# Optimization experiments

Measured on AMD Instinct MI355X. Metric: run time of the kernel, lower is better.

The kernel has to match this reference:

```python
import jax, jax.numpy as jnp
import numpy as np

WS = 7  # window size


def _rel_pos_index(ws):
    coords = np.stack(np.meshgrid(np.arange(ws), np.arange(ws), indexing='ij')).reshape(2, -1)
    rel = (coords[:, :, None] - coords[:, None, :]).transpose(1, 2, 0)  # (N,N,2)
    rel[..., 0] += ws - 1
    rel[..., 1] += ws - 1
    rel[..., 0] *= 2 * ws - 1
    return jnp.asarray(rel.sum(-1))  # (N,N) int


def setup_inputs() -> dict:
    key = jax.random.key(0)
    ks = jax.random.split(key, 10)
    B, DIM, H, W, NH = 16, 256, 56, 56, 8
    HD = DIM // NH
    x = jax.random.normal(ks[0], (B, DIM, H, W), jnp.float32)
    qkv_w = jax.random.normal(ks[1], (DIM, 3 * DIM), jnp.float32) * 0.02
    qkv_b = jnp.zeros((3 * DIM,), jnp.float32)
    fc_w = jax.random.normal(ks[2], (9, 3 * NH), jnp.float32) * 0.1
    fc_b = jnp.zeros((9,), jnp.float32)
    base = np.zeros((9, 3, 3), np.float32)
    for i in range(9):
        base[i, i // 3, i % 3] = 1.0
    dep_w = jnp.asarray(np.broadcast_to(base, (DIM, 9, 3, 3)).copy()) \
        + jax.random.normal(ks[3], (DIM, 9, 3, 3), jnp.float32) * 0.01
    proj_w = jax.random.normal(ks[4], (DIM, DIM), jnp.float32) * 0.02
    proj_b = jnp.zeros((DIM,), jnp.float32)
    rpb_table = jax.random.normal(ks[5], ((2 * WS - 1) * (2 * WS - 1), NH), jnp.float32) * 0.02
    rate1 = jnp.full((1,), 0.5, jnp.float32)
    rate2 = jnp.full((1,), 0.5, jnp.float32)
    return dict(x=x, qkv_w=qkv_w, qkv_b=qkv_b, fc_w=fc_w, fc_b=fc_b, dep_w=dep_w,
                proj_w=proj_w, proj_b=proj_b, rpb_table=rpb_table, rate1=rate1, rate2=rate2)


def reference(x, qkv_w, qkv_b, fc_w, fc_b, dep_w, proj_w, proj_b, rpb_table, rate1, rate2):
    B, DIM, H, W = x.shape
    NH = fc_w.shape[1] // 3
    HD = DIM // NH
    N = WS * WS
    xp = jnp.transpose(x, (0, 2, 3, 1))              # (B,H,W,C)
    qkv = xp @ qkv_w + qkv_b                          # (B,H,W,3C)

    # ----- conv branch -----
    f_all = qkv.reshape(B, H * W, 3 * NH, HD)         # (B,HW,3NH,HD)
    fc_out = jnp.einsum('oc,bncd->bnod', fc_w, f_all) + fc_b[None, None, :, None]  # (B,HW,9,HD)
    # torch channel layout: (B, HD, 9, HW) -> (B, 9*HD, H, W) with hd-major ordering
    f_conv = jnp.transpose(fc_out, (0, 3, 2, 1)).reshape(B, 9 * HD, H, W)
    out_conv = jax.lax.conv_general_dilated(
        f_conv, dep_w, window_strides=(1, 1), padding=((1, 1), (1, 1)),
        feature_group_count=HD, dimension_numbers=('NCHW', 'OIHW', 'NCHW'))  # (B,C,H,W)
    out_conv = jnp.transpose(out_conv, (0, 2, 3, 1))  # (B,H,W,C)

    # ----- window attention branch -----
    w = qkv.reshape(B, H // WS, WS, W // WS, WS, 3 * DIM)
    w = jnp.transpose(w, (0, 1, 3, 2, 4, 5)).reshape(-1, N, 3 * DIM)  # (B_,N,3C)
    B_ = w.shape[0]
    w = w.reshape(B_, N, 3, NH, HD)
    q, k, v = jnp.transpose(w, (2, 0, 3, 1, 4))       # each (B_,NH,N,HD)
    scale = HD ** -0.5
    attn = jnp.einsum('bhnd,bhmd->bhnm', q * scale, k)  # (B_,NH,N,N)
    idx = _rel_pos_index(WS)
    bias = jnp.transpose(rpb_table[idx.reshape(-1)].reshape(N, N, NH), (2, 0, 1))  # (NH,N,N)
    attn = jax.nn.softmax(attn + bias[None], axis=-1)
    o = jnp.einsum('bhnm,bhmd->bnhd', attn, v).reshape(B_, N, DIM)
    o = o @ proj_w.T + proj_b                          # torch Linear: y = x W^T + b
    o = o.reshape(B_, WS, WS, DIM)
    o = o.reshape(B, H // WS, W // WS, WS, WS, DIM)
    o = jnp.transpose(o, (0, 1, 3, 2, 4, 5)).reshape(B, H, W, DIM)

    out = rate1 * o + rate2 * out_conv
    return jnp.transpose(out, (0, 3, 1, 2))           # (B,C,H,W)
```

## Files before the change

kernel.cpp:

```cpp
#include <hip/hip_runtime.h>

#define BATCH 16
#define DIM 256
#define HH 56
#define WW 56
#define HWP 3136
#define M_TOT 50176
#define NQKV 768
#define NHEADS 8
#define HDIM 32
#define NWIN 49
#define QKV_BYTES   77070336ull
#define XT_OFF      77070336ull
#define XT_BYTES    25690112ull
#define WQT_OFF    102760448ull
#define PWB_OFF    103153664ull
#define FCONV_OFF  103284736ull

typedef float f32x4 __attribute__((ext_vector_type(4)));
typedef short short8 __attribute__((ext_vector_type(8)));
typedef unsigned short ushort4v __attribute__((ext_vector_type(4)));

__device__ __forceinline__ short f2bf(float f) {
    unsigned u = __float_as_uint(f);
    u += 0x7fffu + ((u >> 16) & 1u);
    return (short)(u >> 16);
}
__device__ __forceinline__ float bf2f(unsigned short u) {
    return __uint_as_float(((unsigned)u) << 16);
}
__device__ __forceinline__ unsigned pack2bf(float lo, float hi) {
    unsigned ul = __float_as_uint(lo); ul += 0x7fffu + ((ul >> 16) & 1u);
    unsigned uh = __float_as_uint(hi); uh += 0x7fffu + ((uh >> 16) & 1u);
    return (ul >> 16) | (uh & 0xffff0000u);
}
__device__ __forceinline__ int div7(int n) { return (n * 9363) >> 16; }

__global__ __launch_bounds__(256) void xpose_kernel(const float* __restrict__ x,
                                                    unsigned short* __restrict__ xt) {
    __shared__ unsigned short tls[64 * 448];
    const int tid = threadIdx.x;
    const int p0 = blockIdx.x * 448;
    const int k0 = blockIdx.y * 64;
    const int b  = blockIdx.z;
    const float* xb = x + ((size_t)b * DIM + k0) * HWP + p0;
    #pragma unroll
    for (int pass = 0; pass < 28; ++pass) {
        int idx = tid + pass * 256;
        int ch = idx / 112, px4 = idx - ch * 112;
        float4 v = *(const float4*)(xb + (size_t)ch * HWP + px4 * 4);
        int px4s = px4 ^ ((ch >> 3) & 7);
        ushort4v s;
        s[0] = (unsigned short)f2bf(v.x); s[1] = (unsigned short)f2bf(v.y);
        s[2] = (unsigned short)f2bf(v.z); s[3] = (unsigned short)f2bf(v.w);
        *(ushort4v*)&tls[ch * 448 + px4s * 4] = s;
    }
    __syncthreads();
    unsigned short* xto = xt + ((size_t)b * HWP + p0) * DIM + k0;
    #pragma unroll
    for (int q = 0; q < 14; ++q) {
        int idx = tid + q * 256;
        int px = idx >> 3, j8 = (idx & 7) * 8;
        int key = (j8 >> 3) & 7;
        int pxs = ((px >> 2) ^ key) * 4 + (px & 3);
        unsigned r[4];
        #pragma unroll
        for (int jj = 0; jj < 4; ++jj) {
            unsigned lo = tls[(j8 + 2 * jj) * 448 + pxs];
            unsigned hi = tls[(j8 + 2 * jj + 1) * 448 + pxs];
            r[jj] = lo | (hi << 16);
        }
        uint4 o; o.x = r[0]; o.y = r[1]; o.z = r[2]; o.w = r[3];
        *(uint4*)(xto + (size_t)px * DIM + j8) = o;
    }
}

__global__ __launch_bounds__(256) void prep_kernel(const float* __restrict__ wq,
                                                   const float* __restrict__ pw,
                                                   unsigned short* __restrict__ wqt,
                                                   unsigned short* __restrict__ pwb) {
    const int tid = threadIdx.x;
    const int bid = blockIdx.x;
    if (bid < 48) {
        __shared__ float t[64][65];
        const int j0 = (bid >> 2) * 64, k0 = (bid & 3) * 64;
        #pragma unroll
        for (int kk = tid >> 6; kk < 64; kk += 4)
            t[kk][tid & 63] = wq[(size_t)(k0 + kk) * NQKV + j0 + (tid & 63)];
        __syncthreads();
        const int jj = tid >> 2, c16 = (tid & 3) * 16;
        unsigned short* dst = wqt + (size_t)(j0 + jj) * DIM + k0 + c16;
        #pragma unroll
        for (int i = 0; i < 16; ++i) dst[i] = (unsigned short)f2bf(t[c16 + i][jj]);
    } else {
        const int base = (bid - 48) * 4096 + tid;
        #pragma unroll
        for (int i = 0; i < 16; ++i)
            pwb[base + i * 256] = (unsigned short)f2bf(pw[base + i * 256]);
    }
}

__global__ __launch_bounds__(256) void qkv_gemm(const unsigned short* __restrict__ xt,
                                                const unsigned short* __restrict__ wqt,
                                                const float* __restrict__ bq,
                                                unsigned short* __restrict__ qkv) {
    __shared__ short A_lds[128 * 64];
    __shared__ short B_lds[128 * 64];
    const int bidx = blockIdx.x;
    const int wg = (bidx & 7) * 294 + (bidx >> 3);
    const int jt = wg % 6, mt = wg / 6;
    const int m0 = mt * 128, j0 = jt * 128;

    const int tid = threadIdx.x;
    const int lane = tid & 63;
    const int wave = tid >> 6;
    const int wr = wave >> 1, wc = wave & 1;

    const int srow = tid & 127;
    const int kh = tid >> 7;
    const unsigned short* aptr = xt  + (size_t)(m0 + srow) * DIM + kh * 32;
    const unsigned short* bptr = wqt + (size_t)(j0 + srow) * DIM + kh * 32;

    f32x4 acc[4][4];
    #pragma unroll
    for (int i = 0; i < 4; ++i)
        #pragma unroll
        for (int j = 0; j < 4; ++j) acc[i][j] = (f32x4){0.f, 0.f, 0.f, 0.f};

    const int r = lane & 15, q = lane >> 4;
    for (int k0 = 0; k0 < DIM; k0 += 64) {
        __syncthreads();
        #pragma unroll
        for (int g = 0; g < 4; ++g) {
            *(short8*)&A_lds[srow * 64 + 8 * ((kh * 4 + g) ^ (srow & 7))] =
                *(const short8*)(aptr + k0 + g * 8);
            *(short8*)&B_lds[srow * 64 + 8 * ((kh * 4 + g) ^ (srow & 7))] =
                *(const short8*)(bptr + k0 + g * 8);
        }
        __syncthreads();
        #pragma unroll
        for (int ks = 0; ks < 2; ++ks) {
            short8 af[4], bfr[4];
            #pragma unroll
            for (int f = 0; f < 4; ++f) {
                int mrow = wr * 64 + f * 16 + r;
                af[f] = *(const short8*)&A_lds[mrow * 64 + 8 * ((ks * 4 + q) ^ (mrow & 7))];
                int nrow = wc * 64 + f * 16 + r;
                bfr[f] = *(const short8*)&B_lds[nrow * 64 + 8 * ((ks * 4 + q) ^ (nrow & 7))];
            }
            #pragma unroll
            for (int fm = 0; fm < 4; ++fm)
                #pragma unroll
                for (int fj = 0; fj < 4; ++fj)
                    acc[fm][fj] = __builtin_amdgcn_mfma_f32_16x16x32_bf16(
                        af[fm], bfr[fj], acc[fm][fj], 0, 0, 0);
        }
    }
    #pragma unroll
    for (int fm = 0; fm < 4; ++fm) {
        const int mbase = m0 + wr * 64 + fm * 16 + q * 4;
        #pragma unroll
        for (int fj = 0; fj < 4; ++fj) {
            const int j = j0 + wc * 64 + fj * 16 + r;
            const float bias = bq[j];
            unsigned short* op = qkv + (size_t)mbase * NQKV + j;
            #pragma unroll
            for (int rg = 0; rg < 4; ++rg)
                op[(size_t)rg * NQKV] = (unsigned short)f2bf(acc[fm][fj][rg] + bias);
        }
    }
}

__global__ __launch_bounds__(256) void fc_kernel(const unsigned short* __restrict__ qkv,
                                                 const float* __restrict__ fc_w,
                                                 const float* __restrict__ fc_b,
                                                 unsigned short* __restrict__ fconv) {
    __shared__ unsigned short f[16 * 768];
    __shared__ float ob[16][289];
    __shared__ float w[9][24];
    __shared__ float bsh[9];
    const int tid = threadIdx.x;
    if (tid < 216) w[tid / 24][tid % 24] = fc_w[tid];
    if (tid < 9) bsh[tid] = fc_b[tid];
    const int p0 = blockIdx.x * 16;
    const int b  = blockIdx.y;
    const uint4* src = (const uint4*)(qkv + ((size_t)b * HWP + p0) * NQKV);
    uint4* dstf = (uint4*)f;
    #pragma unroll
    for (int i = 0; i < 6; ++i) dstf[tid + i * 256] = src[tid + i * 256];
    __syncthreads();
    #pragma unroll
    for (int it = 0; it < 2; ++it) {
        const int item = tid + it * 256;
        const int pp = item >> 5, g = item & 31;
        const unsigned short* fr = f + pp * 768 + g;
        float acc[9];
        #pragma unroll
        for (int o = 0; o < 9; ++o) acc[o] = bsh[o];
        #pragma unroll
        for (int c = 0; c < 24; ++c) {
            float v = bf2f(fr[c * 32]);
            #pragma unroll
            for (int o = 0; o < 9; ++o) acc[o] += w[o][c] * v;
        }
        #pragma unroll
        for (int o = 0; o < 9; ++o) ob[pp][g * 9 + o] = acc[o];
    }
    __syncthreads();
    unsigned short* og = fconv + (size_t)b * 288 * HWP + p0;
    for (int i = tid; i < 288 * 16; i += 256) {
        int ch = i >> 4, pp = i & 15;
        og[(size_t)ch * HWP + pp] = (unsigned short)f2bf(ob[pp][ch]);
    }
}

__global__ __launch_bounds__(256) void conv_kernel(const unsigned short* __restrict__ fconv,
                                                   const float* __restrict__ dep_w,
                                                   const float* __restrict__ rate2p,
                                                   float* __restrict__ out) {
    __shared__ unsigned short hal[9][10][64];
    __shared__ float wfl[81][8];
    const int tid = threadIdx.x;
    const int strip = blockIdx.x;
    const int g = blockIdx.y, b = blockIdx.z;

    for (int i = tid; i < 648; i += 256) {
        int ok = i >> 3, c8 = i & 7;
        wfl[ok][c8] = dep_w[(size_t)(g * 8 + c8) * 81 + ok];
    }
    const unsigned short* fp = fconv + ((size_t)b * 288 + g * 9) * HWP;
    const int y0 = strip * 8 - 1;
    for (int i = tid; i < 5760; i += 256) {
        int col = i & 63;
        int rest = i >> 6;
        int o = rest / 10, y = rest - o * 10;
        int gy = y0 + y, gx = col - 1;
        unsigned short v = 0;
        if (gy >= 0 && gy < HH && (unsigned)gx < WW)
            v = fp[(size_t)o * HWP + gy * WW + gx];
        hal[o][y][col] = v;
    }
    __syncthreads();

    const int x = tid & 63;
    const int w = tid >> 6;
    const int e = x & ~1;
    const bool odd = (x & 1) != 0;
    float acc[2][8] = {};
    for (int o = 0; o < 9; ++o) {
        float V[4][3];
        #pragma unroll
        for (int h = 0; h < 4; ++h) {
            const unsigned short* hr = &hal[o][2 * w + h][e];
            unsigned D0 = *(const unsigned*)hr;
            unsigned D1 = *(const unsigned*)(hr + 2);
            float a0 = __uint_as_float(D0 << 16);
            float a1 = __uint_as_float(D0 & 0xffff0000u);
            float a2 = __uint_as_float(D1 << 16);
            float a3 = __uint_as_float(D1 & 0xffff0000u);
            V[h][0] = odd ? a1 : a0;
            V[h][1] = odd ? a2 : a1;
            V[h][2] = odd ? a3 : a2;
        }
        #pragma unroll
        for (int ky = 0; ky < 3; ++ky)
            #pragma unroll
            for (int kx = 0; kx < 3; ++kx) {
                f32x4 w0 = *(const f32x4*)&wfl[o * 9 + ky * 3 + kx][0];
                f32x4 w1 = *(const f32x4*)&wfl[o * 9 + ky * 3 + kx][4];
                #pragma unroll
                for (int j = 0; j < 2; ++j) {
                    const float vv = V[j + ky][kx];
                    acc[j][0] += vv * w0[0]; acc[j][1] += vv * w0[1];
                    acc[j][2] += vv * w0[2]; acc[j][3] += vv * w0[3];
                    acc[j][4] += vv * w1[0]; acc[j][5] += vv * w1[1];
                    acc[j][6] += vv * w1[2]; acc[j][7] += vv * w1[3];
                }
            }
    }
    if (x < WW) {
        const float r2 = rate2p[0];
        #pragma unroll
        for (int j = 0; j < 2; ++j) {
            const int y = strip * 8 + 2 * w + j;
            #pragma unroll
            for (int c8 = 0; c8 < 8; ++c8)
                out[((size_t)b * DIM + g * 8 + c8) * HWP + y * WW + x] = r2 * acc[j][c8];
        }
    }
}

__global__ __launch_bounds__(512) void attn_kernel(const unsigned short* __restrict__ qkv,
                                                   const float* __restrict__ rpb,
                                                   unsigned short* __restrict__ obuf) {
    __shared__ __attribute__((aligned(16))) short VT[256 * 72];
    __shared__ __attribute__((aligned(16))) short PL[8 * 16 * 72];
    const int tid = threadIdx.x;
    const int win = blockIdx.x;
    const int b = win >> 6, wrw = win & 63;
    const int wy = wrw >> 3, wx = wrw & 7;
    const size_t wbase = (size_t)b * HWP + (size_t)(wy * 7) * WW + wx * 7;

    {
        const int m = tid & 63;
        const int mq = div7(m), mr = m - mq * 7;
        const unsigned short* vrow = qkv + (wbase + mq * WW + mr) * NQKV + 512;
        for (int R = tid >> 6; R < 256; R += 8)
            VT[R * 72 + m] = (m < 49) ? (short)vrow[R] : (short)0;
    }

    const int lane = tid & 63;
    const int h = tid >> 6;
    const int c = lane & 15, qg = lane >> 4;

    short8 aq[4], bk[4];
    #pragma unroll
    for (int f = 0; f < 4; ++f) {
        int t = f * 16 + c; if (t > 48) t = 48;
        const int tq = div7(t), tr = t - tq * 7;
        const unsigned short* base = qkv + (wbase + tq * WW + tr) * NQKV + h * 32 + qg * 8;
        aq[f] = *(const short8*)base;
        bk[f] = *(const short8*)(base + 256);
    }
    __syncthreads();

    short8 bv[2][2];
    #pragma unroll
    for (int ks = 0; ks < 2; ++ks)
        #pragma unroll
        for (int fo = 0; fo < 2; ++fo)
            bv[ks][fo] = *(const short8*)&VT[(h * 32 + fo * 16 + c) * 72 + ks * 32 + qg * 8];

    const float scale = 0.17677669529663687f;
    short* pw = PL + h * 16 * 72;

    #pragma unroll
    for (int fm = 0; fm < 4; ++fm) {
        f32x4 s[4];
        #pragma unroll
        for (int fj = 0; fj < 4; ++fj)
            s[fj] = __builtin_amdgcn_mfma_f32_16x16x32_bf16(aq[fm], bk[fj],
                                                            (f32x4){0.f,0.f,0.f,0.f}, 0, 0, 0);
        float p[4][4];
        #pragma unroll
        for (int reg = 0; reg < 4; ++reg) {
            int n = fm * 16 + qg * 4 + reg; int nc = n > 48 ? 48 : n;
            int nd = div7(nc), nm = nc - nd * 7;
            #pragma unroll
            for (int fj = 0; fj < 4; ++fj) {
                int mm = fj * 16 + c;
                float bias;
                if (mm < 49) {
                    int md = div7(mm), mmod = mm - md * 7;
                    int idx = (nd - md + 6) * 13 + (nm - mmod + 6);
                    bias = rpb[idx * NHEADS + h];
                } else bias = -1e30f;
                p[fj][reg] = s[fj][reg] * scale + bias;
            }
        }
        float inv[4];
        #pragma unroll
        for (int reg = 0; reg < 4; ++reg) {
            float mx = fmaxf(fmaxf(p[0][reg], p[1][reg]), fmaxf(p[2][reg], p[3][reg]));
            mx = fmaxf(mx, __shfl_xor(mx, 1));
            mx = fmaxf(mx, __shfl_xor(mx, 2));
            mx = fmaxf(mx, __shfl_xor(mx, 4));
            mx = fmaxf(mx, __shfl_xor(mx, 8));
            float sum = 0.f;
            #pragma unroll
            for (int fj = 0; fj < 4; ++fj) {
                float e = __expf(p[fj][reg] - mx);
                p[fj][reg] = e; sum += e;
            }
            sum += __shfl_xor(sum, 1);
            sum += __shfl_xor(sum, 2);
            sum += __shfl_xor(sum, 4);
            sum += __shfl_xor(sum, 8);
            inv[reg] = 1.0f / sum;
        }
        #pragma unroll
        for (int fj = 0; fj < 4; ++fj)
            #pragma unroll
            for (int reg = 0; reg < 4; ++reg) {
                float v = p[fj][reg] * inv[reg];
                float o = __shfl_xor(v, 1);
                unsigned packed = (c & 1) ? pack2bf(o, v) : pack2bf(v, o);
                if ((c & 1) == 0)
                    *(unsigned*)&pw[(qg * 4 + reg) * 72 + fj * 16 + c] = packed;
            }
        short8 ap0 = *(const short8*)&pw[c * 72 + 0 * 32 + qg * 8];
        short8 ap1 = *(const short8*)&pw[c * 72 + 1 * 32 + qg * 8];
        #pragma unroll
        for (int fo = 0; fo < 2; ++fo) {
            f32x4 o4 = __builtin_amdgcn_mfma_f32_16x16x32_bf16(ap0, bv[0][fo],
                                                               (f32x4){0.f,0.f,0.f,0.f}, 0, 0, 0);
            o4 = __builtin_amdgcn_mfma_f32_16x16x32_bf16(ap1, bv[1][fo], o4, 0, 0, 0);
            #pragma unroll
            for (int reg = 0; reg < 4; ++reg) {
                int n = fm * 16 + qg * 4 + reg;
                if (n < 49) {
                    int nd = div7(n), nm = n - nd * 7;
                    obuf[(wbase + nd * WW + nm) * DIM + h * 32 + fo * 16 + c] =
                        (unsigned short)f2bf(o4[reg]);
                }
            }
        }
    }
}

__global__ __launch_bounds__(256) void proj_gemm(const unsigned short* __restrict__ obuf,
                                                 const unsigned short* __restrict__ pwb,
                                                 const float* __restrict__ pb,
                                                 const float* __restrict__ rate1p,
                                                 float* __restrict__ out) {
    __shared__ short M_lds[128 * 64];
    __shared__ short C_lds[128 * 64];
    const int bidx = blockIdx.x;
    const int wg = (bidx & 7) * 98 + (bidx >> 3);
    const int ct = wg & 1, mt = wg >> 1;
    const int m0 = mt * 128, c0 = ct * 128;

    const int tid = threadIdx.x;
    const int lane = tid & 63;
    const int wave = tid >> 6;
    const int wr = wave >> 1, wc = wave & 1;

    const int srow = tid & 127;
    const int kh = tid >> 7;
    const unsigned short* mptr = obuf + (size_t)(m0 + srow) * DIM + kh * 32;
    const unsigned short* cptr = pwb  + (size_t)(c0 + srow) * DIM + kh * 32;

    f32x4 acc[4][4];
    #pragma unroll
    for (int i = 0; i < 4; ++i)
        #pragma unroll
        for (int j = 0; j < 4; ++j) acc[i][j] = (f32x4){0.f, 0.f, 0.f, 0.f};

    const int r = lane & 15, q = lane >> 4;
    for (int k0 = 0; k0 < DIM; k0 += 64) {
        __syncthreads();
        #pragma unroll
        for (int g = 0; g < 4; ++g) {
            *(short8*)&M_lds[srow * 64 + 8 * ((kh * 4 + g) ^ (srow & 7))] =
                *(const short8*)(mptr + k0 + g * 8);
            *(short8*)&C_lds[srow * 64 + 8 * ((kh * 4 + g) ^ (srow & 7))] =
                *(const short8*)(cptr + k0 + g * 8);
        }
        __syncthreads();
        #pragma unroll
        for (int ks = 0; ks < 2; ++ks) {
            short8 cf[4], mf[4];
            #pragma unroll
            for (int f = 0; f < 4; ++f) {
                int crow = wr * 64 + f * 16 + r;
                cf[f] = *(const short8*)&C_lds[crow * 64 + 8 * ((ks * 4 + q) ^ (crow & 7))];
                int mrow = wc * 64 + f * 16 + r;
                mf[f] = *(const short8*)&M_lds[mrow * 64 + 8 * ((ks * 4 + q) ^ (mrow & 7))];
            }
            #pragma unroll
            for (int fc = 0; fc < 4; ++fc)
                #pragma unroll
                for (int fm2 = 0; fm2 < 4; ++fm2)
                    acc[fc][fm2] = __builtin_amdgcn_mfma_f32_16x16x32_bf16(
                        cf[fc], mf[fm2], acc[fc][fm2], 0, 0, 0);
        }
    }
    const float r1 = rate1p[0];
    size_t boff[4];
    #pragma unroll
    for (int fm2 = 0; fm2 < 4; ++fm2) {
        int mb = m0 + wc * 64 + fm2 * 16 + r;
        boff[fm2] = (size_t)(mb / HWP) * DIM * HWP + (mb % HWP);
    }
    #pragma unroll
    for (int fc = 0; fc < 4; ++fc) {
        #pragma unroll
        for (int reg = 0; reg < 4; ++reg) {
            const int cc = c0 + wr * 64 + fc * 16 + q * 4 + reg;
            const float bias = pb[cc];
            #pragma unroll
            for (int fm2 = 0; fm2 < 4; ++fm2) {
                float* dst = out + boff[fm2] + (size_t)cc * HWP;
                *dst = *dst + r1 * (acc[fc][fm2][reg] + bias);
            }
        }
    }
}

extern "C" void kernel_launch(void* const* d_in, const int* in_sizes, int n_in,
                              void* d_out, int out_size, void* d_ws, size_t ws_size,
                              hipStream_t stream) {
    const float* x      = (const float*)d_in[0];
    const float* qkv_w  = (const float*)d_in[1];
    const float* qkv_b  = (const float*)d_in[2];
    const float* fc_w   = (const float*)d_in[3];
    const float* fc_b   = (const float*)d_in[4];
    const float* dep_w  = (const float*)d_in[5];
    const float* proj_w = (const float*)d_in[6];
    const float* proj_b = (const float*)d_in[7];
    const float* rpb    = (const float*)d_in[8];
    const float* rate1  = (const float*)d_in[9];
    const float* rate2  = (const float*)d_in[10];
    float* out = (float*)d_out;

    unsigned short* qkv   = (unsigned short*)d_ws;
    unsigned short* xt    = (unsigned short*)((char*)d_ws + XT_OFF);
    unsigned short* wqt   = (unsigned short*)((char*)d_ws + WQT_OFF);
    unsigned short* pwb   = (unsigned short*)((char*)d_ws + PWB_OFF);
    unsigned short* fconv = (unsigned short*)((char*)d_ws + FCONV_OFF);
    unsigned short* obuf  = fconv;

    xpose_kernel<<<dim3(7, 4, BATCH), 256, 0, stream>>>(x, xt);
    prep_kernel<<<dim3(64), 256, 0, stream>>>(qkv_w, proj_w, wqt, pwb);
    qkv_gemm<<<dim3(2352), 256, 0, stream>>>(xt, wqt, qkv_b, qkv);
    fc_kernel<<<dim3(HWP / 16, BATCH), 256, 0, stream>>>(qkv, fc_w, fc_b, fconv);
    conv_kernel<<<dim3(7, 32, BATCH), 256, 0, stream>>>(fconv, dep_w, rate2, out);
    attn_kernel<<<dim3(1024), 512, 0, stream>>>(qkv, rpb, obuf);
    proj_gemm<<<dim3(784), 256, 0, stream>>>(obuf, pwb, proj_b, rate1, out);
}
```

Baseline: 284.9 us.

## Load GEMM operands directly to registers, precompute bias table, drop attn LDS staging

The QKV GEMM no longer stages A/B tiles through LDS with barriers. Each wave loads its MFMA fragments straight from global memory into two register buffers and alternates between them in a software pipeline. The prep kernel now builds a dense per-head relative-position bias table, so attention no longer does div7 index math and gathers from the small table. Attention also reads V fragments directly from global memory as scalar gathers instead of through a transposed LDS copy. The trade-off is more redundant, less coalesced global loads and higher register pressure, in exchange for removing LDS traffic and synchronisation.

Result: no change. 289.5 us (+1.6%).

```diff
diff --git a/kernel.cpp b/kernel.cpp
--- a/kernel.cpp
+++ b/kernel.cpp
@@ -16,6 +16,7 @@
 #define WQT_OFF    102760448ull
 #define PWB_OFF    103153664ull
 #define FCONV_OFF  103284736ull
+#define BIAS_OFF   132186112ull
 
 typedef float f32x4 __attribute__((ext_vector_type(4)));
 typedef short short8 __attribute__((ext_vector_type(8)));
@@ -77,8 +78,10 @@
 
 __global__ __launch_bounds__(256) void prep_kernel(const float* __restrict__ wq,
                                                    const float* __restrict__ pw,
+                                                   const float* __restrict__ rpb,
                                                    unsigned short* __restrict__ wqt,
-                                                   unsigned short* __restrict__ pwb) {
+                                                   unsigned short* __restrict__ pwb,
+                                                   float* __restrict__ biasT) {
     const int tid = threadIdx.x;
     const int bid = blockIdx.x;
     if (bid < 48) {
@@ -92,11 +95,25 @@
         unsigned short* dst = wqt + (size_t)(j0 + jj) * DIM + k0 + c16;
         #pragma unroll
         for (int i = 0; i < 16; ++i) dst[i] = (unsigned short)f2bf(t[c16 + i][jj]);
-    } else {
+    } else if (bid < 64) {
         const int base = (bid - 48) * 4096 + tid;
         #pragma unroll
         for (int i = 0; i < 16; ++i)
             pwb[base + i * 256] = (unsigned short)f2bf(pw[base + i * 256]);
+    } else {
+        const int h = bid - 64;
+        #pragma unroll
+        for (int i = 0; i < 16; ++i) {
+            int idx = tid + i * 256;
+            int n = idx >> 6, m = idx & 63;
+            float v = -1e30f;
+            if (n < 49 && m < 49) {
+                int nd = div7(n), md = div7(m);
+                int ii = (nd - md + 6) * 13 + ((n - nd * 7) - (m - md * 7) + 6);
+                v = rpb[ii * NHEADS + h];
+            }
+            biasT[h * 4096 + idx] = v;
+        }
     }
 }
 
@@ -104,8 +121,6 @@
                                                 const unsigned short* __restrict__ wqt,
                                                 const float* __restrict__ bq,
                                                 unsigned short* __restrict__ qkv) {
-    __shared__ short A_lds[128 * 64];
-    __shared__ short B_lds[128 * 64];
     const int bidx = blockIdx.x;
     const int wg = (bidx & 7) * 294 + (bidx >> 3);
     const int jt = wg % 6, mt = wg / 6;
@@ -115,11 +130,15 @@
     const int lane = tid & 63;
     const int wave = tid >> 6;
     const int wr = wave >> 1, wc = wave & 1;
-
-    const int srow = tid & 127;
-    const int kh = tid >> 7;
-    const unsigned short* aptr = xt  + (size_t)(m0 + srow) * DIM + kh * 32;
-    const unsigned short* bptr = wqt + (size_t)(j0 + srow) * DIM + kh * 32;
+    const int r = lane & 15, q = lane >> 4;
+
+    const unsigned short* ap[4];
+    const unsigned short* bp[4];
+    #pragma unroll
+    for (int f = 0; f < 4; ++f) {
+        ap[f] = xt  + (size_t)(m0 + wr * 64 + f * 16 + r) * DIM + q * 8;
+        bp[f] = wqt + (size_t)(j0 + wc * 64 + f * 16 + r) * DIM + q * 8;
+    }
 
     f32x4 acc[4][4];
     #pragma unroll
@@ -127,35 +146,56 @@
         #pragma unroll
         for (int j = 0; j < 4; ++j) acc[i][j] = (f32x4){0.f, 0.f, 0.f, 0.f};
 
-    const int r = lane & 15, q = lane >> 4;
-    for (int k0 = 0; k0 < DIM; k0 += 64) {
-        __syncthreads();
-        #pragma unroll
-        for (int g = 0; g < 4; ++g) {
-            *(short8*)&A_lds[srow * 64 + 8 * ((kh * 4 + g) ^ (srow & 7))] =
-                *(const short8*)(aptr + k0 + g * 8);
-            *(short8*)&B_lds[srow * 64 + 8 * ((kh * 4 + g) ^ (srow & 7))] =
-                *(const short8*)(bptr + k0 + g * 8);
-        }
-        __syncthreads();
-        #pragma unroll
-        for (int ks = 0; ks < 2; ++ks) {
-            short8 af[4], bfr[4];
-            #pragma unroll
-            for (int f = 0; f < 4; ++f) {
-                int mrow = wr * 64 + f * 16 + r;
-                af[f] = *(const short8*)&A_lds[mrow * 64 + 8 * ((ks * 4 + q) ^ (mrow & 7))];
-                int nrow = wc * 64 + f * 16 + r;
-                bfr[f] = *(const short8*)&B_lds[nrow * 64 + 8 * ((ks * 4 + q) ^ (nrow & 7))];
-            }
+    short8 A0[4][2], B0[4][2], A1[4][2], B1[4][2];
+
+    auto LOAD0 = [&](int K0) {
+        #pragma unroll
+        for (int f = 0; f < 4; ++f) {
+            A0[f][0] = *(const short8*)(ap[f] + K0);
+            A0[f][1] = *(const short8*)(ap[f] + K0 + 32);
+            B0[f][0] = *(const short8*)(bp[f] + K0);
+            B0[f][1] = *(const short8*)(bp[f] + K0 + 32);
+        }
+    };
+    auto LOAD1 = [&](int K0) {
+        #pragma unroll
+        for (int f = 0; f < 4; ++f) {
+            A1[f][0] = *(const short8*)(ap[f] + K0);
+            A1[f][1] = *(const short8*)(ap[f] + K0 + 32);
+            B1[f][0] = *(const short8*)(bp[f] + K0);
+            B1[f][1] = *(const short8*)(bp[f] + K0 + 32);
+        }
+    };
+    auto STEP0 = [&]() {
+        #pragma unroll
+        for (int ks = 0; ks < 2; ++ks)
             #pragma unroll
             for (int fm = 0; fm < 4; ++fm)
                 #pragma unroll
                 for (int fj = 0; fj < 4; ++fj)
                     acc[fm][fj] = __builtin_amdgcn_mfma_f32_16x16x32_bf16(
-                        af[fm], bfr[fj], acc[fm][fj], 0, 0, 0);
-        }
-    }
+                        A0[fm][ks], B0[fj][ks], acc[fm][fj], 0, 0, 0);
+    };
+    auto STEP1 = [&]() {
+        #pragma unroll
+        for (int ks = 0; ks < 2; ++ks)
+            #pragma unroll
+            for (int fm = 0; fm < 4; ++fm)
+                #pragma unroll
+                for (int fj = 0; fj < 4; ++fj)
+                    acc[fm][fj] = __builtin_amdgcn_mfma_f32_16x16x32_bf16(
+                        A1[fm][ks], B1[fj][ks], acc[fm][fj], 0, 0, 0);
+    };
+
+    LOAD0(0);
+    LOAD1(64);
+    STEP0();
+    LOAD0(128);
+    STEP1();
+    LOAD1(192);
+    STEP0();
+    STEP1();
+
     #pragma unroll
     for (int fm = 0; fm < 4; ++fm) {
         const int mbase = m0 + wr * 64 + fm * 16 + q * 4;
@@ -291,23 +331,14 @@
 }
 
 __global__ __launch_bounds__(512) void attn_kernel(const unsigned short* __restrict__ qkv,
-                                                   const float* __restrict__ rpb,
+                                                   const float* __restrict__ biasT,
                                                    unsigned short* __restrict__ obuf) {
-    __shared__ __attribute__((aligned(16))) short VT[256 * 72];
     __shared__ __attribute__((aligned(16))) short PL[8 * 16 * 72];
     const int tid = threadIdx.x;
     const int win = blockIdx.x;
     const int b = win >> 6, wrw = win & 63;
     const int wy = wrw >> 3, wx = wrw & 7;
     const size_t wbase = (size_t)b * HWP + (size_t)(wy * 7) * WW + wx * 7;
-
-    {
-        const int m = tid & 63;
-        const int mq = div7(m), mr = m - mq * 7;
-        const unsigned short* vrow = qkv + (wbase + mq * WW + mr) * NQKV + 512;
-        for (int R = tid >> 6; R < 256; R += 8)
-            VT[R * 72 + m] = (m < 49) ? (short)vrow[R] : (short)0;
-    }
 
     const int lane = tid & 63;
     const int h = tid >> 6;
@@ -322,16 +353,21 @@
         aq[f] = *(const short8*)base;
         bk[f] = *(const short8*)(base + 256);
     }
-    __syncthreads();
-
     short8 bv[2][2];
     #pragma unroll
     for (int ks = 0; ks < 2; ++ks)
         #pragma unroll
-        for (int fo = 0; fo < 2; ++fo)
-            bv[ks][fo] = *(const short8*)&VT[(h * 32 + fo * 16 + c) * 72 + ks * 32 + qg * 8];
+        for (int i = 0; i < 8; ++i) {
+            int pix = ks * 32 + qg * 8 + i; if (pix > 48) pix = 48;
+            const int pd = div7(pix);
+            const unsigned short* vp = qkv + (wbase + pd * WW + (pix - pd * 7)) * NQKV
+                                           + 512 + h * 32 + c;
+            bv[ks][0][i] = (short)vp[0];
+            bv[ks][1][i] = (short)vp[16];
+        }
 
     const float scale = 0.17677669529663687f;
+    const float* bt = biasT + h * 4096;
     short* pw = PL + h * 16 * 72;
 
     #pragma unroll
@@ -344,19 +380,10 @@
         float p[4][4];
         #pragma unroll
         for (int reg = 0; reg < 4; ++reg) {
-            int n = fm * 16 + qg * 4 + reg; int nc = n > 48 ? 48 : n;
-            int nd = div7(nc), nm = nc - nd * 7;
-            #pragma unroll
-            for (int fj = 0; fj < 4; ++fj) {
-                int mm = fj * 16 + c;
-                float bias;
-                if (mm < 49) {
-                    int md = div7(mm), mmod = mm - md * 7;
-                    int idx = (nd - md + 6) * 13 + (nm - mmod + 6);
-                    bias = rpb[idx * NHEADS + h];
-                } else bias = -1e30f;
-                p[fj][reg] = s[fj][reg] * scale + bias;
-            }
+            const float* brow = bt + (fm * 16 + qg * 4 + reg) * 64;
+            #pragma unroll
+            for (int fj = 0; fj < 4; ++fj)
+                p[fj][reg] = s[fj][reg] * scale + brow[fj * 16 + c];
         }
         float inv[4];
         #pragma unroll
@@ -508,13 +535,14 @@
     unsigned short* wqt   = (unsigned short*)((char*)d_ws + WQT_OFF);
     unsigned short* pwb   = (unsigned short*)((char*)d_ws + PWB_OFF);
     unsigned short* fconv = (unsigned short*)((char*)d_ws + FCONV_OFF);
+    float*          biasT = (float*)((char*)d_ws + BIAS_OFF);
     unsigned short* obuf  = fconv;
 
     xpose_kernel<<<dim3(7, 4, BATCH), 256, 0, stream>>>(x, xt);
-    prep_kernel<<<dim3(64), 256, 0, stream>>>(qkv_w, proj_w, wqt, pwb);
+    prep_kernel<<<dim3(72), 256, 0, stream>>>(qkv_w, proj_w, rpb, wqt, pwb, biasT);
     qkv_gemm<<<dim3(2352), 256, 0, stream>>>(xt, wqt, qkv_b, qkv);
     fc_kernel<<<dim3(HWP / 16, BATCH), 256, 0, stream>>>(qkv, fc_w, fc_b, fconv);
     conv_kernel<<<dim3(7, 32, BATCH), 256, 0, stream>>>(fconv, dep_w, rate2, out);
-    attn_kernel<<<dim3(1024), 512, 0, stream>>>(qkv, rpb, obuf);
+    attn_kernel<<<dim3(1024), 512, 0, stream>>>(qkv, biasT, obuf);
     proj_gemm<<<dim3(784), 256, 0, stream>>>(obuf, pwb, proj_b, rate1, out);
 }
```
